# Kernel optimization log

Measured on AMD Instinct MI355X. Metric: run time of the kernel, lower is better.

The kernel has to match this reference:

```python
import jax, jax.numpy as jnp
import numpy as np

N, DEG, F_IN, F_OUT = 50000, 16, 128, 128
E = N * DEG


def setup_inputs() -> dict:
    key = jax.random.key(0)
    k1, k2, k3 = jax.random.split(key, 3)
    x = jax.random.normal(k1, (N, F_IN), dtype=jnp.float32)
    # flat ragged neighbor features: edge e belongs to node seg_ids[e]
    neigh = jax.random.normal(k2, (E, F_IN), dtype=jnp.float32)
    seg_ids = (jnp.arange(E, dtype=jnp.int32) // DEG)  # sorted, each node has DEG neighbors
    # nn.Linear(in, out, bias=False) weight: [out_features, in_features]
    W = jax.random.normal(k3, (F_OUT, F_IN), dtype=jnp.float32) / np.sqrt(F_IN)
    return {"x": x, "neigh": neigh, "seg_ids": seg_ids, "W": W}


def reference(x, neigh, seg_ids, W):
    n = x.shape[0]
    # per-node mean of neighbor features (segment mean over ragged lists)
    ones = jnp.ones((neigh.shape[0],), dtype=x.dtype)
    counts = jax.ops.segment_sum(ones, seg_ids, num_segments=n)  # [N]
    f = jax.ops.segment_sum(neigh, seg_ids, num_segments=n) / counts[:, None]  # [N, F_in]
    # shared linear transform (no bias)
    x_out = (x + f) @ W.T          # [N, F_out]
    neigh_out = neigh @ W.T        # [E, F_out] (all ragged neighbor sets, flat)
    return (x_out, neigh_out)
```

## Files before the change

### kernel.cpp

```cpp
#include <hip/hip_runtime.h>
#include <hip/hip_bf16.h>

#define FDIM  128
#define GNODE 8
#define DEGC  16
#define TROWS 128
#define ROWB  256
#define WIMG  (FDIM * ROWB)

typedef __attribute__((ext_vector_type(8))) short   bvec8;
typedef __attribute__((ext_vector_type(8))) __bf16  bf16v8;
typedef __attribute__((ext_vector_type(4))) float   fvec4;

__device__ __forceinline__ fvec4 mfma16(bvec8 a, bvec8 b, fvec4 c) {
    return __builtin_amdgcn_mfma_f32_16x16x32_bf16(
        __builtin_bit_cast(bf16v8, a), __builtin_bit_cast(bf16v8, b), c, 0, 0, 0);
}

__device__ __forceinline__ bvec8 ld8(const char* base, int row, int bir) {
    return *(const bvec8*)(base + row * ROWB + (bir ^ ((row & 7) << 4)));
}

__device__ __forceinline__ bvec8 cvt8(fvec4 lo, fvec4 hi) {
    bf16v8 o;
    o[0] = (__bf16)lo.x; o[1] = (__bf16)lo.y; o[2] = (__bf16)lo.z; o[3] = (__bf16)lo.w;
    o[4] = (__bf16)hi.x; o[5] = (__bf16)hi.y; o[6] = (__bf16)hi.z; o[7] = (__bf16)hi.w;
    return __builtin_bit_cast(bvec8, o);
}

__device__ __forceinline__ bvec8 ldcvt(const float* __restrict__ p) {
    return cvt8(((const fvec4*)p)[0], ((const fvec4*)p)[1]);
}

__global__ void prep_w(const float* __restrict__ W, char* __restrict__ wimg) {
    const int u   = blockIdx.x * 256 + threadIdx.x;
    const int row = u >> 4, sl = u & 15;
    bvec8 o = ldcvt(W + (size_t)row * FDIM + sl * 8);
    *(bvec8*)(wimg + row * ROWB + ((sl * 16) ^ ((row & 7) << 4))) = o;
}

__global__ __launch_bounds__(512, 4)
void gcn_fused(const float* __restrict__ x, const float* __restrict__ neigh,
               const char* __restrict__ wimg,
               float* __restrict__ out_x, float* __restrict__ out_nb)
{
    __shared__ __align__(16) char lds_w[WIMG];

    const int t    = threadIdx.x;
    const int blk  = blockIdx.x;
    const int wave = t >> 6, lane = t & 63;
    const int lr = lane & 15, lg = lane >> 4;

    #pragma unroll
    for (int i = 0; i < 4; ++i) {
        const int off = i * 8192 + wave * 1024 + lane * 16;
        __builtin_amdgcn_global_load_lds((const unsigned int*)(wimg + off),
                                         (unsigned int*)(lds_w + off), 16, 0, 0);
    }

    const float* arow = neigh + ((size_t)blk * TROWS + wave * 16 + lr) * FDIM;
    fvec4 af[8];
    #pragma unroll
    for (int q = 0; q < 8; ++q)
        af[q] = ((const fvec4*)arow)[(q >> 1) * 8 + lg * 2 + (q & 1)];

    const float* xrow = x + ((size_t)(blk * GNODE) + wave) * FDIM;
    fvec4 xf[8];
    #pragma unroll
    for (int q = 0; q < 8; ++q)
        xf[q] = ((const fvec4*)xrow)[(q >> 1) * 8 + lg * 2 + (q & 1)];

    __syncthreads();

    bvec8 afr[4], axf[4];
    #pragma unroll
    for (int ks = 0; ks < 4; ++ks) {
        afr[ks] = cvt8(af[ks * 2], af[ks * 2 + 1]);
        axf[ks] = cvt8(xf[ks * 2], xf[ks * 2 + 1]);
    }

    fvec4 acc[8];
    #pragma unroll
    for (int j = 0; j < 8; ++j) acc[j] = (fvec4){0.f, 0.f, 0.f, 0.f};

    #pragma unroll
    for (int ks = 0; ks < 4; ++ks) {
        const int kb = ks * 64 + lg * 16;
        #pragma unroll
        for (int tn = 0; tn < 8; ++tn) {
            bvec8 b = ld8(lds_w, tn * 16 + lr, kb);
            acc[tn] = mfma16(afr[ks], b, acc[tn]);
        }
    }

    const size_t rbase = (size_t)blk * TROWS + wave * 16 + lg * 4;
    #pragma unroll
    for (int tn = 0; tn < 8; ++tn)
        #pragma unroll
        for (int r = 0; r < 4; ++r)
            out_nb[(rbase + r) * FDIM + tn * 16 + lr] = acc[tn][r];

    float p[8];
    #pragma unroll
    for (int tn = 0; tn < 8; ++tn) {
        float s = acc[tn][0] + acc[tn][1] + acc[tn][2] + acc[tn][3];
        s += __shfl_xor(s, 16);
        s += __shfl_xor(s, 32);
        p[tn] = s * (1.f / 16.f);
    }

    fvec4 accx[8];
    #pragma unroll
    for (int j = 0; j < 8; ++j) accx[j] = (fvec4){0.f, 0.f, 0.f, 0.f};
    #pragma unroll
    for (int ks = 0; ks < 4; ++ks) {
        const int kb = ks * 64 + lg * 16;
        #pragma unroll
        for (int tn = 0; tn < 8; ++tn) {
            bvec8 b = ld8(lds_w, tn * 16 + lr, kb);
            accx[tn] = mfma16(axf[ks], b, accx[tn]);
        }
    }

    if (lg == 0) {
        const size_t node = (size_t)blk * GNODE + wave;
        #pragma unroll
        for (int tn = 0; tn < 8; ++tn)
            out_x[node * FDIM + tn * 16 + lr] = accx[tn][0] + p[tn];
    }
}

extern "C" void kernel_launch(void* const* d_in, const int* in_sizes, int n_in,
                              void* d_out, int out_size, void* d_ws, size_t ws_size,
                              hipStream_t stream) {
    const float* x     = (const float*)d_in[0];
    const float* neigh = (const float*)d_in[1];
    const float* W     = (const float*)d_in[3];

    const int n = in_sizes[0] / FDIM;
    float* out_x  = (float*)d_out;
    float* out_nb = out_x + (size_t)n * FDIM;
    char*  wimg   = (char*)d_ws;

    hipLaunchKernelGGL(prep_w, dim3(8), dim3(256), 0, stream, W, wimg);

    const int blocks = n / GNODE;
    hipLaunchKernelGGL(gcn_fused, dim3(blocks), dim3(512), 0, stream,
                       x, neigh, wimg, out_x, out_nb);
}
```

Before: 168.3 us.

## Use persistent blocks with 13 nodes per wave and batched x-row MFMA

Replaces the one-node-per-wave grid of 6250 blocks with a fixed grid of 512 blocks. Each wave processes 13 consecutive nodes, so the W image is loaded into LDS once per block and reused across many nodes. The x@W product for all 13 nodes is done as one 16-row MFMA tile instead of wasting 15 of 16 rows, and the next node's neighbor rows are prefetched while the current outputs are stored. The risk is less memory-level parallelism and a serial per-wave loop with a data-dependent break, on a workload that is mostly memory-bound streaming.

```diff
diff --git a/kernel.cpp b/kernel.cpp
--- a/kernel.cpp
+++ b/kernel.cpp
@@ -2,11 +2,11 @@
 #include <hip/hip_bf16.h>
 
 #define FDIM  128
-#define GNODE 8
 #define DEGC  16
-#define TROWS 128
 #define ROWB  256
 #define WIMG  (FDIM * ROWB)
+#define NBLK  512
+#define NPW   13
 
 typedef __attribute__((ext_vector_type(8))) short   bvec8;
 typedef __attribute__((ext_vector_type(8))) __bf16  bf16v8;
@@ -42,12 +42,11 @@
 __global__ __launch_bounds__(512, 4)
 void gcn_fused(const float* __restrict__ x, const float* __restrict__ neigh,
                const char* __restrict__ wimg,
-               float* __restrict__ out_x, float* __restrict__ out_nb)
+               float* __restrict__ out_x, float* __restrict__ out_nb, int n)
 {
     __shared__ __align__(16) char lds_w[WIMG];
 
     const int t    = threadIdx.x;
-    const int blk  = blockIdx.x;
     const int wave = t >> 6, lane = t & 63;
     const int lr = lane & 15, lg = lane >> 4;
 
@@ -58,56 +57,28 @@
                                          (unsigned int*)(lds_w + off), 16, 0, 0);
     }
 
-    const float* arow = neigh + ((size_t)blk * TROWS + wave * 16 + lr) * FDIM;
-    fvec4 af[8];
-    #pragma unroll
-    for (int q = 0; q < 8; ++q)
-        af[q] = ((const fvec4*)arow)[(q >> 1) * 8 + lg * 2 + (q & 1)];
+    const int  g     = blockIdx.x * 8 + wave;
+    const long nbase = (long)g * NPW;
 
-    const float* xrow = x + ((size_t)(blk * GNODE) + wave) * FDIM;
+    long xr = nbase + lr; if (xr > n - 1) xr = n - 1;
+    const float* xrow = x + (size_t)xr * FDIM;
     fvec4 xf[8];
     #pragma unroll
     for (int q = 0; q < 8; ++q)
         xf[q] = ((const fvec4*)xrow)[(q >> 1) * 8 + lg * 2 + (q & 1)];
 
+    long n0 = nbase; if (n0 > n - 1) n0 = n - 1;
+    const float* ar = neigh + ((size_t)n0 * DEGC + lr) * FDIM;
+    fvec4 af[8];
+    #pragma unroll
+    for (int q = 0; q < 8; ++q)
+        af[q] = ((const fvec4*)ar)[(q >> 1) * 8 + lg * 2 + (q & 1)];
+
     __syncthreads();
 
-    bvec8 afr[4], axf[4];
+    bvec8 axf[4];
     #pragma unroll
-    for (int ks = 0; ks < 4; ++ks) {
-        afr[ks] = cvt8(af[ks * 2], af[ks * 2 + 1]);
-        axf[ks] = cvt8(xf[ks * 2], xf[ks * 2 + 1]);
-    }
-
-    fvec4 acc[8];
-    #pragma unroll
-    for (int j = 0; j < 8; ++j) acc[j] = (fvec4){0.f, 0.f, 0.f, 0.f};
-
-    #pragma unroll
-    for (int ks = 0; ks < 4; ++ks) {
-        const int kb = ks * 64 + lg * 16;
-        #pragma unroll
-        for (int tn = 0; tn < 8; ++tn) {
-            bvec8 b = ld8(lds_w, tn * 16 + lr, kb);
-            acc[tn] = mfma16(afr[ks], b, acc[tn]);
-        }
-    }
-
-    const size_t rbase = (size_t)blk * TROWS + wave * 16 + lg * 4;
-    #pragma unroll
-    for (int tn = 0; tn < 8; ++tn)
-        #pragma unroll
-        for (int r = 0; r < 4; ++r)
-            out_nb[(rbase + r) * FDIM + tn * 16 + lr] = acc[tn][r];
-
-    float p[8];
-    #pragma unroll
-    for (int tn = 0; tn < 8; ++tn) {
-        float s = acc[tn][0] + acc[tn][1] + acc[tn][2] + acc[tn][3];
-        s += __shfl_xor(s, 16);
-        s += __shfl_xor(s, 32);
-        p[tn] = s * (1.f / 16.f);
-    }
+    for (int ks = 0; ks < 4; ++ks) axf[ks] = cvt8(xf[ks * 2], xf[ks * 2 + 1]);
 
     fvec4 accx[8];
     #pragma unroll
@@ -116,18 +87,69 @@
     for (int ks = 0; ks < 4; ++ks) {
         const int kb = ks * 64 + lg * 16;
         #pragma unroll
-        for (int tn = 0; tn < 8; ++tn) {
-            bvec8 b = ld8(lds_w, tn * 16 + lr, kb);
-            accx[tn] = mfma16(axf[ks], b, accx[tn]);
-        }
+        for (int tn = 0; tn < 8; ++tn)
+            accx[tn] = mfma16(axf[ks], ld8(lds_w, tn * 16 + lr, kb), accx[tn]);
     }
 
-    if (lg == 0) {
-        const size_t node = (size_t)blk * GNODE + wave;
+    for (int k = 0; k < NPW; ++k) {
+        const long node = nbase + k;
+        if (node >= n) break;
+
+        bvec8 afr[4];
+        #pragma unroll
+        for (int ks = 0; ks < 4; ++ks) afr[ks] = cvt8(af[ks * 2], af[ks * 2 + 1]);
+
+        fvec4 acc[8];
+        #pragma unroll
+        for (int j = 0; j < 8; ++j) acc[j] = (fvec4){0.f, 0.f, 0.f, 0.f};
+        #pragma unroll
+        for (int ks = 0; ks < 4; ++ks) {
+            const int kb = ks * 64 + lg * 16;
+            #pragma unroll
+            for (int tn = 0; tn < 8; ++tn)
+                acc[tn] = mfma16(afr[ks], ld8(lds_w, tn * 16 + lr, kb), acc[tn]);
+        }
+
+        float p[8];
+        #pragma unroll
+        for (int tn = 0; tn < 8; ++tn) {
+            float s = acc[tn][0] + acc[tn][1] + acc[tn][2] + acc[tn][3];
+            s += __shfl_xor(s, 16);
+            s += __shfl_xor(s, 32);
+            p[tn] = s * (1.f / 16.f);
+        }
+
+        const int krow = k >> 2, kreg = k & 3;
         #pragma unroll
         for (int tn = 0; tn < 8; ++tn)
-            out_x[node * FDIM + tn * 16 + lr] = accx[tn][0] + p[tn];
+            #pragma unroll
+            for (int r = 0; r < 4; ++r)
+                accx[tn][r] += (lg == krow && r == kreg) ? p[tn] : 0.f;
+
+        if (k + 1 < NPW && node + 1 < n) {
+            const float* arn = neigh + ((size_t)(node + 1) * DEGC + lr) * FDIM;
+            #pragma unroll
+            for (int q = 0; q < 8; ++q)
+                af[q] = ((const fvec4*)arn)[(q >> 1) * 8 + lg * 2 + (q & 1)];
+        }
+
+        const size_t rbase = (size_t)node * DEGC + lg * 4;
+        #pragma unroll
+        for (int tn = 0; tn < 8; ++tn)
+            #pragma unroll
+            for (int r = 0; r < 4; ++r)
+                out_nb[(rbase + r) * FDIM + tn * 16 + lr] = acc[tn][r];
     }
+
+    #pragma unroll
+    for (int tn = 0; tn < 8; ++tn)
+        #pragma unroll
+        for (int r = 0; r < 4; ++r) {
+            const int  row  = lg * 4 + r;
+            const long node = nbase + row;
+            if (row < NPW && node < n)
+                out_x[(size_t)node * FDIM + tn * 16 + lr] = accx[tn][r];
+        }
 }
 
 extern "C" void kernel_launch(void* const* d_in, const int* in_sizes, int n_in,
@@ -144,7 +166,6 @@
 
     hipLaunchKernelGGL(prep_w, dim3(8), dim3(256), 0, stream, W, wimg);
 
-    const int blocks = n / GNODE;
-    hipLaunchKernelGGL(gcn_fused, dim3(blocks), dim3(512), 0, stream,
-                       x, neigh, wimg, out_x, out_nb);
+    hipLaunchKernelGGL(gcn_fused, dim3(NBLK), dim3(512), 0, stream,
+                       x, neigh, wimg, out_x, out_nb, n);
 }
```

Measured after the change: 192.3 us. 1.14x slower.
